# Kernel optimization log

Hardware: AMD Instinct MI355X
Metric: run time of the kernel (lower is better)

The kernel has to match this reference:

```python
import jax, jax.numpy as jnp
import numpy as np

NG, GPG, K = 32, 128, 32           # graphs, nodes per graph per side, neighbors
NB, RMAX, NNEI = 10, 20.0, 32.0    # radial basis, max radius, num_neighbors
CS, CX = float(np.sin(np.pi / 8)), float(np.cos(np.pi / 8))


def _sh(u):
    # real spherical harmonics l=0..3, e3nn 'component' normalization (y-up convention)
    x, y, z = u[:, 0], u[:, 1], u[:, 2]
    s3, s5, s15, s7 = 3 ** 0.5, 5 ** 0.5, 15 ** 0.5, 7 ** 0.5
    x2, y2, z2 = x * x, y * y, z * z
    sh2_0 = s15 * x * z
    sh2_4 = 0.5 * s15 * (z2 - x2)
    sh = [jnp.ones_like(x),
          s3 * x, s3 * y, s3 * z,
          sh2_0, s15 * x * y, s5 * (y2 - 0.5 * (x2 + z2)), s15 * y * z, sh2_4,
          (42 ** 0.5 / 6) * (sh2_0 * z + sh2_4 * x), s7 * sh2_0 * y,
          (168 ** 0.5 / 8) * (4 * y2 - x2 - z2) * x,
          (s7 / 2) * y * (2 * y2 - 3 * x2 - 3 * z2),
          (168 ** 0.5 / 8) * z * (4 * y2 - x2 - z2),
          s7 * sh2_4 * y,
          (42 ** 0.5 / 6) * (sh2_4 * z - sh2_0 * x)]
    return jnp.stack(sh, -1)  # [E,16]


def setup_inputs():
    ks = jax.random.split(jax.random.key(0), 24)
    Nh = NG * GPG
    wt_pos = jax.random.uniform(ks[0], (Nh, 3)) * 10.0
    mt_pos = jax.random.uniform(ks[1], (Nh, 3)) * 10.0
    wt_x = jax.random.normal(ks[2], (Nh, 25))
    mt_x = jax.random.normal(ks[3], (Nh, 25))
    batch = jnp.repeat(jnp.arange(NG, dtype=jnp.int32), GPG)
    # fixed radius-graph surrogate: K random in-graph neighbors per node (src != dst)
    rng = np.random.default_rng(1)
    N = 2 * Nh
    src = np.repeat(np.arange(N), K)
    off = rng.integers(1, GPG, size=N * K)
    dst = (src // GPG) * GPG + (src % GPG + off) % GPG
    p = lambda k, s: jax.random.normal(k, s)
    return {
        'wt_pos': wt_pos, 'mt_pos': mt_pos, 'wt_x': wt_x, 'mt_x': mt_x,
        'wt_batch': batch, 'mt_batch': batch,
        'edge_src': jnp.asarray(src, jnp.int32), 'edge_dst': jnp.asarray(dst, jnp.int32),
        'sc1_w': p(ks[4], (25, 16)), 'lin1a': p(ks[5], (25, 25)),
        'fc1_w1': p(ks[6], (10, 128)), 'fc1_w2': p(ks[7], (128, 100)),
        'l2a0': p(ks[8], (25, 16)), 'l2a1': p(ks[9], (25, 3)),
        'l2a2': p(ks[10], (25, 2)), 'l2a3': p(ks[11], (25, 1)),
        'sc2_w': p(ks[12], (10, 256)),
        'l1b0': p(ks[13], (10, 10)), 'l1b1': p(ks[14], (3, 3)),
        'l1b2': p(ks[15], (2, 2)), 'l1b3': p(ks[16], (1, 1)),
        'fc2_w1': p(ks[17], (10, 128)), 'fc2_w2': p(ks[18], (128, 16)),
        'lin2b': p(ks[19], (16, 256)),
        'head_w': p(ks[20], (256, 2)) * 0.05, 'head_b': jnp.zeros((2,)),
    }


def reference(wt_pos, mt_pos, wt_x, mt_x, wt_batch, mt_batch, edge_src, edge_dst,
              sc1_w, lin1a, fc1_w1, fc1_w2, l2a0, l2a1, l2a2, l2a3,
              sc2_w, l1b0, l1b1, l1b2, l1b3, fc2_w1, fc2_w2, lin2b, head_w, head_b):
    pos = jnp.concatenate([wt_pos, mt_pos], 0)
    x = jnp.concatenate([wt_x, mt_x], 0)
    batch = jnp.concatenate([wt_batch, mt_batch], 0)
    N = pos.shape[0]

    vec = pos[edge_src] - pos[edge_dst]
    r = jnp.linalg.norm(vec, axis=-1)
    sh = _sh(vec / jnp.maximum(r, 1e-9)[:, None])                  # [E,16]
    centers = jnp.linspace(0.0, RMAX, NB)
    step = RMAX / (NB - 1)
    emb = jnp.exp(-(((r[:, None] - centers) / step) ** 2)) * NB ** 0.5  # [E,10]

    seg = lambda m: jax.ops.segment_sum(m, edge_dst, num_segments=N) / NNEI ** 0.5

    # ---- gate convolution (layer 1): 25x0e (x) SH -> 16x0e + 3x1o + 2x2e + 1x3o
    sc1 = x @ sc1_w / 5.0                                          # self-connection (scalars only)
    h = x @ lin1a / 5.0
    w1 = (jax.nn.silu(emb @ fc1_w1 / NB ** 0.5) @ fc1_w2 / 128 ** 0.5).reshape(-1, 4, 25)
    xs = h[edge_src]                                               # [E,25]
    m0 = seg(xs * w1[:, 0])                                        # [N,25]
    m1 = seg((xs * w1[:, 1])[:, :, None] * sh[:, None, 1:4])       # [N,25,3]
    m2 = seg((xs * w1[:, 2])[:, :, None] * sh[:, None, 4:9])       # [N,25,5]
    m3 = seg((xs * w1[:, 3])[:, :, None] * sh[:, None, 9:16])      # [N,25,7]
    a0 = m0 @ l2a0 / 5.0                                           # [N,16]
    a1 = jnp.einsum('num,uv->nvm', m1, l2a1) / 5.0                 # [N,3,3]
    a2 = jnp.einsum('num,uv->nvm', m2, l2a2) / 5.0                 # [N,2,5]
    a3 = jnp.einsum('num,uv->nvm', m3, l2a3) / 5.0                 # [N,1,7]
    s0 = CS * sc1 + CX * a0                                        # alpha-mix on masked (scalar) channels
    scal = jax.nn.silu(s0[:, :10])
    gates = jax.nn.sigmoid(s0[:, 10:16])
    g1 = a1 * gates[:, 0:3, None]
    g2 = a2 * gates[:, 3:5, None]
    g3 = a3 * gates[:, 5:6, None]

    # ---- output convolution: (10x0e+3x1o+2x2e+1x3o) (x) SH -> 256x0e via l(x)l->0 paths
    sc2 = scal @ sc2_w / 10 ** 0.5
    h0 = scal @ l1b0 / 10 ** 0.5
    h1 = jnp.einsum('num,uv->nvm', g1, l1b1) / 3 ** 0.5
    h2 = jnp.einsum('num,uv->nvm', g2, l1b2) / 2 ** 0.5
    h3 = jnp.einsum('num,uv->nvm', g3, l1b3)
    w2 = jax.nn.silu(emb @ fc2_w1 / NB ** 0.5) @ fc2_w2 / 128 ** 0.5   # [E,16]
    e0 = h0[edge_src] * w2[:, :10]
    e1 = jnp.einsum('eum,em->eu', h1[edge_src], sh[:, 1:4]) / 3 ** 0.5 * w2[:, 10:13]
    e2 = jnp.einsum('eum,em->eu', h2[edge_src], sh[:, 4:9]) / 5 ** 0.5 * w2[:, 13:15]
    e3 = jnp.einsum('eum,em->eu', h3[edge_src], sh[:, 9:16]) / 7 ** 0.5 * w2[:, 15:16]
    mid = seg(jnp.concatenate([e0, e1, e2, e3], -1))               # [N,16]
    y = CS * sc2 + CX * (mid @ lin2b / 4.0)                        # [N,256]

    # ---- per-graph mean pool (== torch boolean-mask loop) + head
    ssum = jax.ops.segment_sum(y, batch, num_segments=NG)
    cnt = jax.ops.segment_sum(jnp.ones((N, 1), y.dtype), batch, num_segments=NG)
    out = (ssum / cnt) @ head_w + head_b                           # [NG,2]
    return out[:, 0].astype(jnp.float32), out[:, 1].astype(jnp.float32)
```

## Files before the change

### kernel.cpp

```cpp
#include <hip/hip_runtime.h>

typedef unsigned int uint;

#define NH_   4096
#define NNODE 8192
#define NEDGE 262144
#define TS    4096
#define RT    17.4f
#define RIDX  (((float)(TS - 1)) / RT)

#define OFF_H      0
#define OFF_SC1    229376
#define OFF_SCALS  655360
#define OFF_MIDS   655680
#define OFF_TABU   656384
#define OFF_SSRC   1278976
#define OFF_SOFF   1541120

template <int I> struct ic { static constexpr int v = I; };
template <int N, typename F>
__device__ __forceinline__ void UN(F&& f) {
  if constexpr (N > 0) { UN<N - 1>(f); f(ic<N - 1>{}); }
}

template <int K>
__device__ __forceinline__ float f4c(float4 v) {
  if constexpr (K == 0) return v.x;
  else if constexpr (K == 1) return v.y;
  else if constexpr (K == 2) return v.z;
  else return v.w;
}
template <int C>
__device__ __forceinline__ float f4get(const float4* v) {
  return f4c<C & 3>(v[C >> 2]);
}
template <int K>
__device__ __forceinline__ uint u4c(uint4 v) {
  if constexpr (K == 0) return v.x;
  else if constexpr (K == 1) return v.y;
  else if constexpr (K == 2) return v.z;
  else return v.w;
}
template <int CH>
__device__ __forceinline__ float upk(const uint4* wr) {
  constexpr int pr = CH >> 1;
  uint u = u4c<pr & 3>(wr[pr >> 2]);
  if constexpr (CH & 1) return __uint_as_float(u & 0xffff0000u);
  else return __uint_as_float(u << 16);
}

__device__ __forceinline__ float sigmoidf_(float v) { return 1.0f / (1.0f + __expf(-v)); }

template <int C, int B>
__device__ __forceinline__ void cred_rec(float* a, int lane) {
  if constexpr ((1 << B) < C) {
    const bool hi = (lane >> B) & 1;
    constexpr int n = C >> (B + 1);
    UN<n>([&](auto j){
      float s0 = a[2 * j.v], s1 = a[2 * j.v + 1];
      float send = hi ? s0 : s1;
      float recv = __shfl_xor(send, 1 << B);
      a[j.v] = (hi ? s1 : s0) + recv;
    });
    cred_rec<C, B + 1>(a, lane);
  }
}
template <int C>
__device__ __forceinline__ float creduce(float* v, int lane) {
  cred_rec<C, 0>(v, lane);
  float s = v[0];
#pragma unroll
  for (int m = C; m < 64; m <<= 1) s += __shfl_xor(s, m);
  return s;
}
template <int B>
__device__ __forceinline__ void cred32_rec(float* a, int lane) {
  if constexpr (B < 5) {
    const bool hi = (lane >> B) & 1;
    constexpr int n = 64 >> (B + 1);
    UN<n>([&](auto j){
      float s0 = a[2 * j.v], s1 = a[2 * j.v + 1];
      float send = hi ? s0 : s1;
      float recv = __shfl_xor(send, 1 << B);
      a[j.v] = (hi ? s1 : s0) + recv;
    });
    cred32_rec<B + 1>(a, lane);
  }
}

__device__ __forceinline__ void make_emb(float r, float* embs) {
  float rb = r * 0.45f;
  UN<10>([&](auto b){ float d = rb - (float)b.v; embs[b.v] = __expf(-d * d); });
}

__device__ __forceinline__ void make_sh(float vx, float vy, float vz, float r, float* sh) {
  float rinv = 1.0f / fmaxf(r, 1e-9f);
  float x = vx * rinv, y = vy * rinv, z = vz * rinv;
  float x2 = x * x, y2 = y * y, z2 = z * z;
  float shA = 3.87298334620742f * x * z;
  float shB = 1.93649167310371f * (z2 - x2);
  sh[0] = 1.f;
  sh[1] = 1.73205080756888f * x;
  sh[2] = 1.73205080756888f * y;
  sh[3] = 1.73205080756888f * z;
  sh[4] = shA;
  sh[5] = 3.87298334620742f * x * y;
  sh[6] = 2.23606797749979f * (y2 - 0.5f * (x2 + z2));
  sh[7] = 3.87298334620742f * y * z;
  sh[8] = shB;
  sh[9]  = 1.08012344973464f * (shA * z + shB * x);
  sh[10] = 2.64575131106459f * shA * y;
  sh[11] = 1.62018517460197f * (4.f * y2 - x2 - z2) * x;
  sh[12] = 1.32287565553230f * y * (2.f * y2 - 3.f * x2 - 3.f * z2);
  sh[13] = 1.62018517460197f * z * (4.f * y2 - x2 - z2);
  sh[14] = 2.64575131106459f * shB * y;
  sh[15] = 1.08012344973464f * (shB * z - shA * x);
}

__global__ void __launch_bounds__(256, 4) k_prep(
    const float* __restrict__ wt_x, const float* __restrict__ mt_x,
    const float* __restrict__ lin1a, const float* __restrict__ sc1w,
    const float* __restrict__ fc1w1, const float* __restrict__ fc1w2,
    const float* __restrict__ fc2w1, const float* __restrict__ fc2w2,
    const int* __restrict__ edst,
    float* __restrict__ h, float* __restrict__ sc1,
    uint* __restrict__ tabU, float* __restrict__ zacc,
    int* __restrict__ ssrc, int* __restrict__ soff)
{
  __shared__ float smemf[512];
  const int blk = blockIdx.x;
  const int tid = threadIdx.x;

  if (blk < 2048) {
    float (*sv)[2][128] = (float(*)[2][128])smemf;
    const int lane = tid & 63;
    const int wv = tid >> 6;
    const int si = wv >> 1;
    const int role = wv & 1;
    const int s = blk * 2 + si;
    const float r = (float)s * (RT / (float)(TS - 1));
    float emb[10];
    make_emb(r, emb);
    const float FS1 = 0.003125f;
    const float FS2 = 0.015625f;

    const float* wmat = (role == 0) ? fc1w1 : fc2w1;
    UN<2>([&](auto hh){
      int kk = lane + hh.v * 64;
      float hk = 0.f;
      UN<10>([&](auto j){ hk = fmaf(emb[j.v], wmat[j.v * 128 + kk], hk); });
      sv[si][role][kk] = hk * sigmoidf_(hk);
    });
    __syncthreads();

    float acc = 0.f;
    if (role == 0) {
      const float* base = fc1w2 + lane;
#pragma unroll 4
      for (int k = 0; k < 128; ++k)
        acc = fmaf(sv[si][0][k], base[k * 100], acc);
      acc *= FS1;
    } else {
      const bool isW1 = lane < 36;
      const bool isW2 = (lane >= 36) && (lane < 52);
      if (isW1 || isW2) {
        const float* base = isW1 ? (fc1w2 + 64 + lane) : (fc2w2 + (lane - 36));
        const int stride = isW1 ? 100 : 16;
        const int svi = isW1 ? 0 : 1;
#pragma unroll 4
        for (int k = 0; k < 128; ++k)
          acc = fmaf(sv[si][svi][k], base[k * stride], acc);
        acc *= (isW1 ? FS1 : FS2);
      }
    }

    int srcLo = 0, srcHi = 0;
    bool valid = false;
    if (role == 0) {
      srcLo = 2 * lane; srcHi = srcLo + 1; valid = lane < 32;
    } else {
      if (lane >= 32 && lane < 50)      { int i = lane - 32; srcLo = 2 * i;      srcHi = 2 * i + 1;  valid = true; }
      else if (lane >= 52 && lane < 60) { int i = lane - 52; srcLo = 36 + 2 * i; srcHi = 37 + 2 * i; valid = true; }
    }
    float lo = __shfl(acc, srcLo);
    float hi = __shfl(acc, srcHi);
    if (valid) {
      uint u = ((__float_as_uint(lo) + 0x8000u) >> 16)
             | (((__float_as_uint(hi) + 0x8000u) >> 16) << 16);
      tabU[(size_t)s * 64 + lane] = u;
    }
  } else if (blk < 2080) {
    int i = (blk - 2048) * 256 + tid;
    const float* xp = (i < NH_) ? (wt_x + i * 25) : (mt_x + (i - NH_) * 25);
    float xr[25];
    UN<25>([&](auto m){ xr[m.v] = xp[m.v]; });
    float ah[25], as[16];
    UN<25>([&](auto j){ ah[j.v] = 0.f; });
    UN<16>([&](auto j){ as[j.v] = 0.f; });
    UN<25>([&](auto m){
      float xm = xr[m.v];
      UN<25>([&](auto j){ ah[j.v] = fmaf(xm, lin1a[m.v * 25 + j.v], ah[j.v]); });
      UN<16>([&](auto j){ as[j.v] = fmaf(xm, sc1w[m.v * 16 + j.v], as[j.v]); });
    });
    UN<25>([&](auto j){ h[i * 28 + j.v] = 0.2f * ah[j.v]; });
    UN<16>([&](auto j){ sc1[i * 16 + j.v] = 0.2f * as[j.v]; });
  } else if (blk < 2144) {
    int* hist = (int*)smemf;
    int* cnt  = hist + 128;
    const int g = blk - 2080;
    if (tid < 128) hist[tid] = 0;
    __syncthreads();
    int dl[16];
    UN<16>([&](auto k){
      int e = g * 4096 + k.v * 256 + tid;
      dl[k.v] = edst[e] & 127;
      atomicAdd(&hist[dl[k.v]], 1);
    });
    __syncthreads();
    if (tid < 64) {
      int s0 = hist[2 * tid], s1 = hist[2 * tid + 1];
      int ps = s0 + s1;
      int sum = ps;
#pragma unroll
      for (int m = 1; m < 64; m <<= 1) {
        int t = __shfl_up(sum, m);
        if (tid >= m) sum += t;
      }
      int excl = sum - ps;
      cnt[2 * tid] = excl;
      cnt[2 * tid + 1] = excl + s0;
      soff[g * 128 + 2 * tid] = g * 4096 + excl;
      soff[g * 128 + 2 * tid + 1] = g * 4096 + excl + s0;
    }
    if (g == 0 && tid == 255) soff[NNODE] = NEDGE;
    __syncthreads();
    UN<16>([&](auto k){
      int e = g * 4096 + k.v * 256 + tid;
      int slot = atomicAdd(&cnt[dl[k.v]], 1);
      ssrc[g * 4096 + slot] = e >> 5;
    });
  } else {
    for (int z = tid; z < 832; z += 256) zacc[z] = 0.f;
  }
}

__global__ void __launch_bounds__(256, 3) k_mega(
    const float* __restrict__ wt_pos, const float* __restrict__ mt_pos,
    const int* __restrict__ soff, const int* __restrict__ ssrc,
    const int* __restrict__ edst,
    const uint* __restrict__ tabU, const float* __restrict__ h,
    const float* __restrict__ sc1,
    const float* __restrict__ l2a0, const float* __restrict__ l2a1,
    const float* __restrict__ l2a2, const float* __restrict__ l2a3,
    const float* __restrict__ l1b0, const float* __restrict__ l1b1,
    const float* __restrict__ l1b2, const float* __restrict__ l1b3,
    float* __restrict__ scalsum, float* __restrict__ midsum)
{
  __shared__ float Atile[8][44];
  __shared__ float nodeHs[8][36];

  const int tid = threadIdx.x;
  const int lane = tid & 63;
  const int li = lane & 31;
  const int hw = tid >> 5;
  const int dst = blockIdx.x * 8 + hw;

  {
    const int start = soff[dst];
    const int n = soff[dst + 1] - start;
    const float* pd = (dst < NH_) ? (wt_pos + dst * 3) : (mt_pos + (dst - NH_) * 3);
    const float pdx = pd[0], pdy = pd[1], pdz = pd[2];

    float acc[42];
    UN<42>([&](auto c){ acc[c.v] = 0.f; });

    const int nmax = max(n, __shfl_xor(n, 32));
#pragma unroll 1
    for (int it = 0; it < nmax; it += 32) {
      const int i = it + li;
      if (i < n) {
        const int src = ssrc[start + i];
        const float* ps = (src < NH_) ? (wt_pos + src * 3) : (mt_pos + (src - NH_) * 3);
        float vx = ps[0] - pdx, vy = ps[1] - pdy, vz = ps[2] - pdz;
        float r = sqrtf(vx * vx + vy * vy + vz * vz);
        int ti = min((int)(r * RIDX + 0.5f), TS - 1);
        const uint4* w4 = (const uint4*)(tabU + (size_t)ti * 64);
        uint4 wr[13];
        UN<13>([&](auto j){ wr[j.v] = w4[j.v]; });
        const float4* hp = (const float4*)(h + src * 28);
        float4 hq[7];
        UN<7>([&](auto j){ hq[j.v] = hp[j.v]; });
        float sh[16];
        make_sh(vx, vy, vz, r, sh);

        UN<25>([&](auto mm){
          float t = f4get<mm.v>(hq) * upk<mm.v>(wr);
          UN<16>([&](auto v){ acc[v.v] = fmaf(t, l2a0[mm.v * 16 + v.v], acc[v.v]); });
        });
        {
          float p1[3] = {0.f, 0.f, 0.f};
          UN<25>([&](auto mm){
            float t = f4get<mm.v>(hq) * upk<25 + mm.v>(wr);
            UN<3>([&](auto v){ p1[v.v] = fmaf(t, l2a1[mm.v * 3 + v.v], p1[v.v]); });
          });
          UN<3>([&](auto v){
            UN<3>([&](auto m){ acc[16 + v.v * 3 + m.v] = fmaf(p1[v.v], sh[1 + m.v], acc[16 + v.v * 3 + m.v]); });
          });
        }
        {
          float p2[2] = {0.f, 0.f};
          UN<25>([&](auto mm){
            float t = f4get<mm.v>(hq) * upk<50 + mm.v>(wr);
            UN<2>([&](auto v){ p2[v.v] = fmaf(t, l2a2[mm.v * 2 + v.v], p2[v.v]); });
          });
          UN<2>([&](auto v){
            UN<5>([&](auto m){ acc[25 + v.v * 5 + m.v] = fmaf(p2[v.v], sh[4 + m.v], acc[25 + v.v * 5 + m.v]); });
          });
        }
        {
          float p3 = 0.f;
          UN<25>([&](auto mm){
            float t = f4get<mm.v>(hq) * upk<75 + mm.v>(wr);
            p3 = fmaf(t, l2a3[mm.v], p3);
          });
          UN<7>([&](auto m){ acc[35 + m.v] = fmaf(p3, sh[9 + m.v], acc[35 + m.v]); });
        }
      }
    }

    float red[64];
    UN<42>([&](auto c){ red[c.v] = acc[c.v]; });
    UN<22>([&](auto c){ red[42 + c.v] = 0.f; });
    cred32_rec<0>(red, lane);
    Atile[hw][li] = red[0];
    if (li < 10) Atile[hw][32 + li] = red[1];
  }
  __syncthreads();

  if (tid < 8) {
    const int i = blockIdx.x * 8 + tid;
    float Ai[42];
    UN<42>([&](auto c){ Ai[c.v] = Atile[tid][c.v]; });
    const float CS_ = 0.38268343236509f, CX_ = 0.92387953251129f;
    float scal[10], gate[6];
    UN<10>([&](auto c){
      float s = CS_ * sc1[i * 16 + c.v] + CX_ * Ai[c.v];
      scal[c.v] = s * sigmoidf_(s);
    });
    UN<6>([&](auto c){
      float s = CS_ * sc1[i * 16 + 10 + c.v] + CX_ * Ai[10 + c.v];
      gate[c.v] = sigmoidf_(s);
    });
    UN<10>([&](auto v){
      float a = 0.f;
      UN<10>([&](auto u){ a = fmaf(scal[u.v], l1b0[u.v * 10 + v.v], a); });
      nodeHs[tid][v.v] = a * 0.31622776601684f;
    });
    UN<3>([&](auto v){
      UN<3>([&](auto m){
        float a = 0.f;
        UN<3>([&](auto u){ a = fmaf(Ai[16 + u.v * 3 + m.v] * gate[u.v], l1b1[u.v * 3 + v.v], a); });
        nodeHs[tid][10 + v.v * 3 + m.v] = a * 0.57735026918963f;
      });
    });
    UN<2>([&](auto v){
      UN<5>([&](auto m){
        float a = 0.f;
        UN<2>([&](auto u){ a = fmaf(Ai[25 + u.v * 5 + m.v] * gate[3 + u.v], l1b2[u.v * 2 + v.v], a); });
        nodeHs[tid][19 + v.v * 5 + m.v] = a * 0.70710678118655f;
      });
    });
    float b3 = l1b3[0];
    UN<7>([&](auto m){ nodeHs[tid][29 + m.v] = Ai[35 + m.v] * gate[5] * b3; });

    const int g = (i >> 7) & 31;
    UN<10>([&](auto c){ atomicAdd(&scalsum[g * 10 + c.v], scal[c.v]); });
  }
  __syncthreads();

  {
    const int e = blockIdx.x * 256 + tid;
    const int sl = tid >> 5;
    const int src = blockIdx.x * 8 + sl;
    const int dst2 = edst[e];
    const float* ps = (src < NH_) ? (wt_pos + src * 3) : (mt_pos + (src - NH_) * 3);
    const float* pdp = (dst2 < NH_) ? (wt_pos + dst2 * 3) : (mt_pos + (dst2 - NH_) * 3);
    float vx = ps[0] - pdp[0], vy = ps[1] - pdp[1], vz = ps[2] - pdp[2];
    float r = sqrtf(vx * vx + vy * vy + vz * vz);
    int ti = min((int)(r * RIDX + 0.5f), TS - 1);
    const uint4* w4 = (const uint4*)(tabU + (size_t)ti * 64 + 52);
    uint4 wr[2];
    wr[0] = w4[0]; wr[1] = w4[1];
    float acc[16];
    UN<16>([&](auto c){ acc[c.v] = upk<c.v>(wr); });

    float sh[16];
    make_sh(vx, vy, vz, r, sh);

    const float* Hs = nodeHs[sl];
    float ev[16];
    UN<10>([&](auto c){ ev[c.v] = Hs[c.v] * acc[c.v]; });
    UN<3>([&](auto u){
      float d = 0.f;
      UN<3>([&](auto m){ d = fmaf(Hs[10 + u.v * 3 + m.v], sh[1 + m.v], d); });
      ev[10 + u.v] = d * 0.57735026918963f * acc[10 + u.v];
    });
    UN<2>([&](auto u){
      float d = 0.f;
      UN<5>([&](auto m){ d = fmaf(Hs[19 + u.v * 5 + m.v], sh[4 + m.v], d); });
      ev[13 + u.v] = d * 0.44721359549996f * acc[13 + u.v];
    });
    {
      float d = 0.f;
      UN<7>([&](auto m){ d = fmaf(Hs[29 + m.v], sh[9 + m.v], d); });
      ev[15] = d * 0.37796447300923f * acc[15];
    }

    const int g = (dst2 >> 7) & 31;
    float s = creduce<16>(ev, lane);
    if (lane < 16) atomicAdd(&midsum[g * 16 + lane], s);
  }
}

__global__ void k_final(const float* __restrict__ sc2w, const float* __restrict__ lin2b,
                        const float* __restrict__ headw, const float* __restrict__ headb,
                        const float* __restrict__ scalsum, const float* __restrict__ midsum,
                        float* __restrict__ out)
{
  __shared__ float WA[20];
  __shared__ float WB[32];
  int t = threadIdx.x;
  if (t < 20) {
    int j = t >> 1, o = t & 1;
    float a = 0.f;
    for (int c = 0; c < 256; ++c) a += sc2w[j * 256 + c] * headw[c * 2 + o];
    WA[t] = a;
  } else if (t < 52) {
    int q = t - 20, j = q >> 1, o = q & 1;
    float a = 0.f;
    for (int c = 0; c < 256; ++c) a += lin2b[j * 256 + c] * headw[c * 2 + o];
    WB[q] = a;
  }
  __syncthreads();
  if (t < 64) {
    int g = t & 31, o = t >> 5;
    float a = 0.f;
    for (int j = 0; j < 10; ++j) a += scalsum[g * 10 + j] * WA[j * 2 + o];
    float b = 0.f;
    for (int j = 0; j < 16; ++j) b += midsum[g * 16 + j] * WB[j * 2 + o];
    float y = a * (0.38268343236509f * 0.31622776601684f)
            + b * (0.92387953251129f * 0.25f);
    out[o * 32 + g] = y * (1.0f / 256.0f) + headb[o];
  }
}

extern "C" void kernel_launch(void* const* d_in, const int* in_sizes, int n_in,
                              void* d_out, int out_size, void* d_ws, size_t ws_size,
                              hipStream_t stream)
{
  float* ws = (float*)d_ws;
  const float* wt_pos = (const float*)d_in[0];
  const float* mt_pos = (const float*)d_in[1];
  const float* wt_x   = (const float*)d_in[2];
  const float* mt_x   = (const float*)d_in[3];
  const int* edst     = (const int*)d_in[7];
  const float* sc1w   = (const float*)d_in[8];
  const float* lin1a  = (const float*)d_in[9];
  const float* fc1w1  = (const float*)d_in[10];
  const float* fc1w2  = (const float*)d_in[11];
  const float* l2a0   = (const float*)d_in[12];
  const float* l2a1   = (const float*)d_in[13];
  const float* l2a2   = (const float*)d_in[14];
  const float* l2a3   = (const float*)d_in[15];
  const float* sc2w   = (const float*)d_in[16];
  const float* l1b0   = (const float*)d_in[17];
  const float* l1b1   = (const float*)d_in[18];
  const float* l1b2   = (const float*)d_in[19];
  const float* l1b3   = (const float*)d_in[20];
  const float* fc2w1  = (const float*)d_in[21];
  const float* fc2w2  = (const float*)d_in[22];
  const float* lin2b  = (const float*)d_in[23];
  const float* headw  = (const float*)d_in[24];
  const float* headb  = (const float*)d_in[25];

  float* h       = ws + OFF_H;
  float* sc1     = ws + OFF_SC1;
  float* scalsum = ws + OFF_SCALS;
  float* midsum  = ws + OFF_MIDS;
  uint*  tabU    = (uint*)(ws + OFF_TABU);
  int*   ssrc    = (int*)(ws + OFF_SSRC);
  int*   soff    = (int*)(ws + OFF_SOFF);

  k_prep<<<2145, 256, 0, stream>>>(wt_x, mt_x, lin1a, sc1w, fc1w1, fc1w2, fc2w1, fc2w2,
                                   edst, h, sc1, tabU, scalsum, ssrc, soff);
  k_mega<<<1024, 256, 0, stream>>>(wt_pos, mt_pos, soff, ssrc, edst, tabU, h, sc1,
                                   l2a0, l2a1, l2a2, l2a3,
                                   l1b0, l1b1, l1b2, l1b3,
                                   scalsum, midsum);
  k_final<<<1, 256, 0, stream>>>(sc2w, lin2b, headw, headb, scalsum, midsum, (float*)d_out);
}
```

Measured before the change: 72.08 us.

## Precompute per-edge geometry in prep kernel and remap mega kernel to one wave per node

```diff
diff --git a/kernel.cpp b/kernel.cpp
--- a/kernel.cpp
+++ b/kernel.cpp
@@ -1,4 +1,5 @@
 #include <hip/hip_runtime.h>
+#include <hip/hip_fp16.h>
 
 typedef unsigned int uint;
 
@@ -11,11 +12,12 @@
 
 #define OFF_H      0
 #define OFF_SC1    229376
-#define OFF_SCALS  655360
-#define OFF_MIDS   655680
-#define OFF_TABU   656384
-#define OFF_SSRC   1278976
-#define OFF_SOFF   1541120
+#define OFF_SCALS  360448
+#define OFF_MIDS   360768
+#define OFF_TABU   361280
+#define OFF_SOFF   623424
+#define OFF_EC     631680
+#define OFF_SA     1680256
 
 template <int I> struct ic { static constexpr int v = I; };
 template <int N, typename F>
@@ -73,29 +75,13 @@
   for (int m = C; m < 64; m <<= 1) s += __shfl_xor(s, m);
   return s;
 }
-template <int B>
-__device__ __forceinline__ void cred32_rec(float* a, int lane) {
-  if constexpr (B < 5) {
-    const bool hi = (lane >> B) & 1;
-    constexpr int n = 64 >> (B + 1);
-    UN<n>([&](auto j){
-      float s0 = a[2 * j.v], s1 = a[2 * j.v + 1];
-      float send = hi ? s0 : s1;
-      float recv = __shfl_xor(send, 1 << B);
-      a[j.v] = (hi ? s1 : s0) + recv;
-    });
-    cred32_rec<B + 1>(a, lane);
-  }
-}
 
 __device__ __forceinline__ void make_emb(float r, float* embs) {
   float rb = r * 0.45f;
   UN<10>([&](auto b){ float d = rb - (float)b.v; embs[b.v] = __expf(-d * d); });
 }
 
-__device__ __forceinline__ void make_sh(float vx, float vy, float vz, float r, float* sh) {
-  float rinv = 1.0f / fmaxf(r, 1e-9f);
-  float x = vx * rinv, y = vy * rinv, z = vz * rinv;
+__device__ __forceinline__ void make_sh_n(float x, float y, float z, float* sh) {
   float x2 = x * x, y2 = y * y, z2 = z * z;
   float shA = 3.87298334620742f * x * z;
   float shB = 1.93649167310371f * (z2 - x2);
@@ -117,7 +103,8 @@
   sh[15] = 1.08012344973464f * (shB * z - shA * x);
 }
 
-__global__ void __launch_bounds__(256, 4) k_prep(
+__global__ void __launch_bounds__(512, 2) k_prep(
+    const float* __restrict__ wt_pos, const float* __restrict__ mt_pos,
     const float* __restrict__ wt_x, const float* __restrict__ mt_x,
     const float* __restrict__ lin1a, const float* __restrict__ sc1w,
     const float* __restrict__ fc1w1, const float* __restrict__ fc1w2,
@@ -125,19 +112,20 @@
     const int* __restrict__ edst,
     float* __restrict__ h, float* __restrict__ sc1,
     uint* __restrict__ tabU, float* __restrict__ zacc,
-    int* __restrict__ ssrc, int* __restrict__ soff)
+    uint4* __restrict__ edgeC, uint4* __restrict__ sortedA,
+    int* __restrict__ soff)
 {
-  __shared__ float smemf[512];
+  __shared__ float smemf[1024];
   const int blk = blockIdx.x;
   const int tid = threadIdx.x;
 
-  if (blk < 2048) {
+  if (blk < 1024) {
     float (*sv)[2][128] = (float(*)[2][128])smemf;
     const int lane = tid & 63;
     const int wv = tid >> 6;
     const int si = wv >> 1;
     const int role = wv & 1;
-    const int s = blk * 2 + si;
+    const int s = blk * 4 + si;
     const float r = (float)s * (RT / (float)(TS - 1));
     float emb[10];
     make_emb(r, emb);
@@ -189,8 +177,8 @@
              | (((__float_as_uint(hi) + 0x8000u) >> 16) << 16);
       tabU[(size_t)s * 64 + lane] = u;
     }
-  } else if (blk < 2080) {
-    int i = (blk - 2048) * 256 + tid;
+  } else if (blk < 1040) {
+    int i = (blk - 1024) * 512 + tid;
     const float* xp = (i < NH_) ? (wt_x + i * 25) : (mt_x + (i - NH_) * 25);
     float xr[25];
     UN<25>([&](auto m){ xr[m.v] = xp[m.v]; });
@@ -204,17 +192,31 @@
     });
     UN<25>([&](auto j){ h[i * 28 + j.v] = 0.2f * ah[j.v]; });
     UN<16>([&](auto j){ sc1[i * 16 + j.v] = 0.2f * as[j.v]; });
-  } else if (blk < 2144) {
+  } else if (blk < 1104) {
     int* hist = (int*)smemf;
     int* cnt  = hist + 128;
-    const int g = blk - 2080;
+    const int g = blk - 1040;
     if (tid < 128) hist[tid] = 0;
     __syncthreads();
-    int dl[16];
-    UN<16>([&](auto k){
-      int e = g * 4096 + k.v * 256 + tid;
-      dl[k.v] = edst[e] & 127;
+    int dl[8]; uint gy[8], gz[8];
+    UN<8>([&](auto k){
+      const int e = g * 4096 + k.v * 512 + tid;
+      const int src = e >> 5;
+      const int dst = edst[e];
+      dl[k.v] = dst & 127;
       atomicAdd(&hist[dl[k.v]], 1);
+      const float* ps = (src < NH_) ? (wt_pos + src * 3) : (mt_pos + (src - NH_) * 3);
+      const float* pd = (dst < NH_) ? (wt_pos + dst * 3) : (mt_pos + (dst - NH_) * 3);
+      float vx = ps[0] - pd[0], vy = ps[1] - pd[1], vz = ps[2] - pd[2];
+      float r = sqrtf(vx * vx + vy * vy + vz * vz);
+      int ti = min((int)(r * RIDX + 0.5f), TS - 1);
+      float rinv = 1.0f / fmaxf(r, 1e-9f);
+      uint hx = (uint)__half_as_ushort(__float2half(vx * rinv));
+      uint hy = (uint)__half_as_ushort(__float2half(vy * rinv));
+      uint hz = (uint)__half_as_ushort(__float2half(vz * rinv));
+      gy[k.v] = hx | (hy << 16);
+      gz[k.v] = hz | ((uint)ti << 16);
+      edgeC[e] = make_uint4((uint)dst, gy[k.v], gz[k.v], 0u);
     });
     __syncthreads();
     if (tid < 64) {
@@ -232,22 +234,21 @@
       soff[g * 128 + 2 * tid] = g * 4096 + excl;
       soff[g * 128 + 2 * tid + 1] = g * 4096 + excl + s0;
     }
-    if (g == 0 && tid == 255) soff[NNODE] = NEDGE;
+    if (g == 0 && tid == 511) soff[NNODE] = NEDGE;
     __syncthreads();
-    UN<16>([&](auto k){
-      int e = g * 4096 + k.v * 256 + tid;
+    UN<8>([&](auto k){
+      const int e = g * 4096 + k.v * 512 + tid;
       int slot = atomicAdd(&cnt[dl[k.v]], 1);
-      ssrc[g * 4096 + slot] = e >> 5;
+      sortedA[g * 4096 + slot] = make_uint4((uint)(e >> 5), gy[k.v], gz[k.v], 0u);
     });
   } else {
-    for (int z = tid; z < 832; z += 256) zacc[z] = 0.f;
-  }
-}
-
-__global__ void __launch_bounds__(256, 3) k_mega(
-    const float* __restrict__ wt_pos, const float* __restrict__ mt_pos,
-    const int* __restrict__ soff, const int* __restrict__ ssrc,
-    const int* __restrict__ edst,
+    for (int z = tid; z < 832; z += 512) zacc[z] = 0.f;
+  }
+}
+
+__global__ void __launch_bounds__(256, 4) k_mega(
+    const int* __restrict__ soff, const uint4* __restrict__ sortedA,
+    const uint4* __restrict__ edgeC,
     const uint* __restrict__ tabU, const float* __restrict__ h,
     const float* __restrict__ sc1,
     const float* __restrict__ l2a0, const float* __restrict__ l2a1,
@@ -256,34 +257,31 @@
     const float* __restrict__ l1b2, const float* __restrict__ l1b3,
     float* __restrict__ scalsum, float* __restrict__ midsum)
 {
-  __shared__ float Atile[8][44];
-  __shared__ float nodeHs[8][36];
+  __shared__ float Atile[4][44];
+  __shared__ float nodeHs[4][36];
 
   const int tid = threadIdx.x;
   const int lane = tid & 63;
-  const int li = lane & 31;
-  const int hw = tid >> 5;
-  const int dst = blockIdx.x * 8 + hw;
+  const int wv = tid >> 6;
+  const int dst = blockIdx.x * 4 + wv;
 
   {
     const int start = soff[dst];
     const int n = soff[dst + 1] - start;
-    const float* pd = (dst < NH_) ? (wt_pos + dst * 3) : (mt_pos + (dst - NH_) * 3);
-    const float pdx = pd[0], pdy = pd[1], pdz = pd[2];
 
     float acc[42];
     UN<42>([&](auto c){ acc[c.v] = 0.f; });
 
-    const int nmax = max(n, __shfl_xor(n, 32));
 #pragma unroll 1
-    for (int it = 0; it < nmax; it += 32) {
-      const int i = it + li;
+    for (int it = 0; it < n; it += 64) {
+      const int i = it + lane;
       if (i < n) {
-        const int src = ssrc[start + i];
-        const float* ps = (src < NH_) ? (wt_pos + src * 3) : (mt_pos + (src - NH_) * 3);
-        float vx = ps[0] - pdx, vy = ps[1] - pdy, vz = ps[2] - pdz;
-        float r = sqrtf(vx * vx + vy * vy + vz * vz);
-        int ti = min((int)(r * RIDX + 0.5f), TS - 1);
+        uint4 gg = sortedA[start + i];
+        const int src = (int)gg.x;
+        float x = __half2float(__ushort_as_half((unsigned short)(gg.y & 0xffffu)));
+        float y = __half2float(__ushort_as_half((unsigned short)(gg.y >> 16)));
+        float z = __half2float(__ushort_as_half((unsigned short)(gg.z & 0xffffu)));
+        const int ti = (int)(gg.z >> 16);
         const uint4* w4 = (const uint4*)(tabU + (size_t)ti * 64);
         uint4 wr[13];
         UN<13>([&](auto j){ wr[j.v] = w4[j.v]; });
@@ -291,7 +289,7 @@
         float4 hq[7];
         UN<7>([&](auto j){ hq[j.v] = hp[j.v]; });
         float sh[16];
-        make_sh(vx, vy, vz, r, sh);
+        make_sh_n(x, y, z, sh);
 
         UN<25>([&](auto mm){
           float t = f4get<mm.v>(hq) * upk<mm.v>(wr);
@@ -331,14 +329,13 @@
     float red[64];
     UN<42>([&](auto c){ red[c.v] = acc[c.v]; });
     UN<22>([&](auto c){ red[42 + c.v] = 0.f; });
-    cred32_rec<0>(red, lane);
-    Atile[hw][li] = red[0];
-    if (li < 10) Atile[hw][32 + li] = red[1];
+    float s = creduce<64>(red, lane);
+    if (lane < 42) Atile[wv][lane] = s;
   }
   __syncthreads();
 
-  if (tid < 8) {
-    const int i = blockIdx.x * 8 + tid;
+  if (tid < 4) {
+    const int i = blockIdx.x * 4 + tid;
     float Ai[42];
     UN<42>([&](auto c){ Ai[c.v] = Atile[tid][c.v]; });
     const float CS_ = 0.38268343236509f, CX_ = 0.92387953251129f;
@@ -378,16 +375,15 @@
   }
   __syncthreads();
 
-  {
-    const int e = blockIdx.x * 256 + tid;
+  if (tid < 128) {
+    const int e = blockIdx.x * 128 + tid;
     const int sl = tid >> 5;
-    const int src = blockIdx.x * 8 + sl;
-    const int dst2 = edst[e];
-    const float* ps = (src < NH_) ? (wt_pos + src * 3) : (mt_pos + (src - NH_) * 3);
-    const float* pdp = (dst2 < NH_) ? (wt_pos + dst2 * 3) : (mt_pos + (dst2 - NH_) * 3);
-    float vx = ps[0] - pdp[0], vy = ps[1] - pdp[1], vz = ps[2] - pdp[2];
-    float r = sqrtf(vx * vx + vy * vy + vz * vz);
-    int ti = min((int)(r * RIDX + 0.5f), TS - 1);
+    uint4 gg = edgeC[e];
+    const int dst2 = (int)gg.x;
+    float x = __half2float(__ushort_as_half((unsigned short)(gg.y & 0xffffu)));
+    float y = __half2float(__ushort_as_half((unsigned short)(gg.y >> 16)));
+    float z = __half2float(__ushort_as_half((unsigned short)(gg.z & 0xffffu)));
+    const int ti = (int)(gg.z >> 16);
     const uint4* w4 = (const uint4*)(tabU + (size_t)ti * 64 + 52);
     uint4 wr[2];
     wr[0] = w4[0]; wr[1] = w4[1];
@@ -395,7 +391,7 @@
     UN<16>([&](auto c){ acc[c.v] = upk<c.v>(wr); });
 
     float sh[16];
-    make_sh(vx, vy, vz, r, sh);
+    make_sh_n(x, y, z, sh);
 
     const float* Hs = nodeHs[sl];
     float ev[16];
@@ -488,12 +484,14 @@
   float* scalsum = ws + OFF_SCALS;
   float* midsum  = ws + OFF_MIDS;
   uint*  tabU    = (uint*)(ws + OFF_TABU);
-  int*   ssrc    = (int*)(ws + OFF_SSRC);
   int*   soff    = (int*)(ws + OFF_SOFF);
-
-  k_prep<<<2145, 256, 0, stream>>>(wt_x, mt_x, lin1a, sc1w, fc1w1, fc1w2, fc2w1, fc2w2,
-                                   edst, h, sc1, tabU, scalsum, ssrc, soff);
-  k_mega<<<1024, 256, 0, stream>>>(wt_pos, mt_pos, soff, ssrc, edst, tabU, h, sc1,
+  uint4* edgeC   = (uint4*)(ws + OFF_EC);
+  uint4* sortedA = (uint4*)(ws + OFF_SA);
+
+  k_prep<<<1105, 512, 0, stream>>>(wt_pos, mt_pos, wt_x, mt_x, lin1a, sc1w,
+                                   fc1w1, fc1w2, fc2w1, fc2w2, edst,
+                                   h, sc1, tabU, scalsum, edgeC, sortedA, soff);
+  k_mega<<<2048, 256, 0, stream>>>(soff, sortedA, edgeC, tabU, h, sc1,
                                    l2a0, l2a1, l2a2, l2a3,
                                    l1b0, l1b1, l1b2, l1b3,
                                    scalsum, midsum);
```

Result: slower. 141.7 us (+96.5%).
